# Kernel tuning notes

Measured on AMD Instinct MI355X. Metric: run time of the kernel, lower is better.

Reference implementation:

```python
import jax, jax.numpy as jnp
import numpy as np

B, DM, DC, H = 16384, 1024, 8, 256  # batch, MRI feat dim, clinical feat dim, hidden_dim


def setup_inputs() -> dict:
    key = jax.random.key(0)
    ks = jax.random.split(key, 16)
    f = lambda k, s: jax.random.normal(k, s, dtype=jnp.float32)
    return {
        # encoder outputs (4 MRI modalities @1024-d, clinical @8-d)
        'feat_t1': f(ks[0], (B, DM)), 'feat_t1c': f(ks[1], (B, DM)),
        'feat_t2': f(ks[2], (B, DM)), 'feat_flair': f(ks[3], (B, DM)),
        'feat_cl': f(ks[4], (B, DC)),
        # per-modality projection Linears (MRI ones stacked: same math as 4 separate Linears)
        'Wp_mri': f(ks[5], (4, H, DM)) * 0.02, 'bp_mri': jnp.zeros((4, H), jnp.float32),
        'Wp_cl': f(ks[6], (H, DC)) * 0.02, 'bp_cl': jnp.zeros((H,), jnp.float32),
        # attention MLP: Linear(256,64) -> Tanh -> Linear(64,1)
        'Wa1': f(ks[7], (64, H)) * 0.02, 'ba1': jnp.zeros((64,), jnp.float32),
        'Wa2': f(ks[8], (1, 64)) * 0.02, 'ba2': jnp.zeros((1,), jnp.float32),
        # classifier: 256->128 LN ReLU -> 128->64 LN ReLU -> 64->1 (num_class-1)
        'Wc1': f(ks[9], (128, H)) * 0.02, 'bc1': jnp.zeros((128,), jnp.float32),
        'g1': jnp.ones((128,), jnp.float32), 'be1': jnp.zeros((128,), jnp.float32),
        'Wc2': f(ks[10], (64, 128)) * 0.02, 'bc2': jnp.zeros((64,), jnp.float32),
        'g2': jnp.ones((64,), jnp.float32), 'be2': jnp.zeros((64,), jnp.float32),
        'Wc3': f(ks[11], (1, 64)) * 0.02, 'bc3': jnp.zeros((1,), jnp.float32),
    }


def _ln(x, g, b, eps=1e-5):
    m = jnp.mean(x, axis=-1, keepdims=True)
    v = jnp.var(x, axis=-1, keepdims=True)
    return (x - m) * jax.lax.rsqrt(v + eps) * g + b


def reference(feat_t1, feat_t1c, feat_t2, feat_flair, feat_cl,
              Wp_mri, bp_mri, Wp_cl, bp_cl,
              Wa1, ba1, Wa2, ba2,
              Wc1, bc1, g1, be1, Wc2, bc2, g2, be2, Wc3, bc3):
    mri = jnp.stack([feat_t1, feat_t1c, feat_t2, feat_flair], axis=1)  # [B,4,DM]
    pm = jnp.einsum('bmd,mhd->bmh', mri, Wp_mri) + bp_mri              # [B,4,H] per-modality Linear
    pc = feat_cl @ Wp_cl.T + bp_cl                                     # [B,H]
    proj = jnp.concatenate([pm, pc[:, None, :]], axis=1)               # [B,5,H] == torch.stack(proj_feats, dim=1)
    scores = jnp.tanh(proj @ Wa1.T + ba1) @ Wa2.T + ba2                # [B,5,1]
    attn_weights = jax.nn.softmax(scores, axis=1)                      # softmax over modalities
    fused = jnp.sum(attn_weights * proj, axis=1)                       # [B,H]
    h = jax.nn.relu(_ln(fused @ Wc1.T + bc1, g1, be1))                 # dropout is identity in eval
    h = jax.nn.relu(_ln(h @ Wc2.T + bc2, g2, be2))
    out = h @ Wc3.T + bc3                                              # [B,1]
    return out, attn_weights
```

## Files before the change

### kernel.cpp

```cpp
#include <hip/hip_runtime.h>
#include <math.h>

typedef unsigned short u16;
typedef unsigned int   u32;
typedef __bf16 bf16x8 __attribute__((ext_vector_type(8)));
typedef float  f32x4  __attribute__((ext_vector_type(4)));
typedef u16    u16x8  __attribute__((ext_vector_type(8)));
typedef u16    u16x4  __attribute__((ext_vector_type(4)));

#define B_TOT 16384
#define DM_   1024
#define H_    256

#define WS_SCORES 41943040
#define WS_WP     42270720
#define WS_WA1    44367872
#define WS_WC1    44400640
#define WS_WC2    44466176

__device__ __forceinline__ u16 f2bf(float f){
  __bf16 h = (__bf16)f;
  return __builtin_bit_cast(u16, h);
}
__device__ __forceinline__ float bf2f(u16 h){
  return __builtin_bit_cast(float, ((u32)h) << 16);
}
__device__ __forceinline__ u16x4 cvt4(f32x4 a){
  u16x4 h;
  #pragma unroll
  for (int j = 0; j < 4; j++) h[j] = f2bf(a[j]);
  return h;
}
__device__ __forceinline__ f32x4 mfma16(bf16x8 a, bf16x8 b, f32x4 c){
  return __builtin_amdgcn_mfma_f32_16x16x32_bf16(a, b, c, 0, 0, 0);
}
__device__ __forceinline__ void glds16(const void* g, void* l){
  __builtin_amdgcn_global_load_lds(
      (const __attribute__((address_space(1))) void*)g,
      (__attribute__((address_space(3))) void*)l, 16, 0, 0);
}

__global__ void k0_convert(const float* __restrict__ s0, u16* __restrict__ d0, int n0,
                           const float* __restrict__ s1, u16* __restrict__ d1, int n1,
                           const float* __restrict__ s2, u16* __restrict__ d2, int n2,
                           const float* __restrict__ s3, u16* __restrict__ d3, int n3)
{
  int total4 = (n0 + n1 + n2 + n3) >> 2;
  for (int i = blockIdx.x * blockDim.x + threadIdx.x; i < total4; i += gridDim.x * blockDim.x){
    int e = i << 2;
    const float* s; u16* d; int off;
    if (e < n0)            { s = s0; d = d0; off = e; }
    else if (e < n0+n1)    { s = s1; d = d1; off = e - n0; }
    else if (e < n0+n1+n2) { s = s2; d = d2; off = e - n0 - n1; }
    else                   { s = s3; d = d3; off = e - n0 - n1 - n2; }
    f32x4 f = *(const f32x4*)(s + off);
    *(u16x4*)(d + off) = cvt4(f);
  }
}

__global__ __launch_bounds__(256) void k1b_clin(
    const float* __restrict__ fcl, const float* __restrict__ Wpcl, const float* __restrict__ bpcl,
    const u16* __restrict__ Wa1bf, const float* __restrict__ ba1,
    const float* __restrict__ Wa2, const float* __restrict__ ba2,
    u16* __restrict__ proj, float* __restrict__ scores)
{
  __shared__ u16 pcs[4][16*264];
  const int tid = threadIdx.x, lane = tid & 63, wv = tid >> 6;
  const int l15 = lane & 15, l4 = lane >> 4;
  const int rbase = blockIdx.x * 64 + wv * 16;

  f32x4 wA[4], wB[4];
  f32x4 bp = *(const f32x4*)(bpcl + lane * 4);
  #pragma unroll
  for (int c = 0; c < 4; c++){
    wA[c] = *(const f32x4*)(Wpcl + (lane*4 + c) * 8);
    wB[c] = *(const f32x4*)(Wpcl + (lane*4 + c) * 8 + 4);
  }
  #pragma unroll 4
  for (int r = 0; r < 16; r++){
    int row = rbase + r;
    f32x4 fA = *(const f32x4*)(fcl + (size_t)row * 8);
    f32x4 fB = *(const f32x4*)(fcl + (size_t)row * 8 + 4);
    u16x4 h;
    #pragma unroll
    for (int c = 0; c < 4; c++){
      float v = bp[c] + fA[0]*wA[c][0] + fA[1]*wA[c][1] + fA[2]*wA[c][2] + fA[3]*wA[c][3]
                      + fB[0]*wB[c][0] + fB[1]*wB[c][1] + fB[2]*wB[c][2] + fB[3]*wB[c][3];
      h[c] = f2bf(v);
    }
    *(u16x4*)(proj + (size_t)row * 1280 + 1024 + lane * 4) = h;
    *(u16x4*)(&pcs[wv][r * 264 + lane * 4]) = h;
  }
  f32x4 at[4];
  #pragma unroll
  for (int nf = 0; nf < 4; nf++) at[nf] = f32x4{0.f,0.f,0.f,0.f};
  #pragma unroll
  for (int kk = 0; kk < 8; kk++){
    bf16x8 a = *(const bf16x8*)((const char*)&pcs[wv][0] + l15*528 + kk*64 + l4*16);
    #pragma unroll
    for (int nf = 0; nf < 4; nf++){
      bf16x8 b = *(const bf16x8*)((const char*)Wa1bf + (nf*16 + l15)*512 + kk*64 + l4*16);
      at[nf] = mfma16(a, b, at[nf]);
    }
  }
  float po[4] = {0.f,0.f,0.f,0.f};
  #pragma unroll
  for (int nf = 0; nf < 4; nf++){
    int col = nf*16 + l15;
    float bb = ba1[col], w2 = Wa2[col];
    #pragma unroll
    for (int rg = 0; rg < 4; rg++) po[rg] += tanhf(at[nf][rg] + bb) * w2;
  }
  #pragma unroll
  for (int rg = 0; rg < 4; rg++){
    #pragma unroll
    for (int d = 1; d < 16; d <<= 1) po[rg] += __shfl_xor(po[rg], d);
  }
  if (l15 == 0){
    float b2 = ba2[0];
    #pragma unroll
    for (int rg = 0; rg < 4; rg++)
      scores[(size_t)(rbase + l4*4 + rg) * 5 + 4] = po[rg] + b2;
  }
}

__global__ __launch_bounds__(512, 6) void k1_proj(
    const float* __restrict__ ft1, const float* __restrict__ ft1c,
    const float* __restrict__ ft2, const float* __restrict__ ftfl,
    const u16* __restrict__ Wpbf, const float* __restrict__ bpm,
    const u16* __restrict__ Wa1bf, const float* __restrict__ ba1,
    const float* __restrict__ Wa2, const float* __restrict__ ba2,
    u16* __restrict__ proj, float* __restrict__ scores)
{
  extern __shared__ char lds[];
  const int bid = blockIdx.x;
  const int mm = (bid & 7) >> 1;
  const int bx = ((bid >> 3) << 1) | (bid & 1);
  const int b0 = bx * 64;
  const int tid = threadIdx.x;
  const int lane = tid & 63;
  const int wv = tid >> 6;
  const int wm = wv >> 2, wn = wv & 3;
  const int l15 = lane & 15, l4 = lane >> 4;

  const float* Am = (mm == 0) ? ft1 : ((mm == 1) ? ft1c : ((mm == 2) ? ft2 : ftfl));
  const char*  Wm = (const char*)(Wpbf + (size_t)mm * (H_ * DM_));
  const char*  Ab8 = (const char*)Am;

  const int a_r = tid >> 3, a_c = tid & 7;
  const size_t a_src0 = (size_t)(b0 + a_r) * 4096 + (size_t)((a_c*16) ^ ((a_r & 7) << 4));
  const int a_dstw = (tid >> 6) * 1024;
  int w_pr[2], w_c[2]; size_t w_src0[2];
  #pragma unroll
  for (int i = 0; i < 2; i++){
    int q = i*512 + tid; w_pr[i] = q >> 3; w_c[i] = q & 7;
    int zp = (w_c[i]*16) ^ ((w_pr[i] & 7) << 4);
    int col = 2*w_pr[i] + (zp >> 6);
    w_src0[i] = (size_t)col * 2048 + (size_t)(zp & 63);
  }

  f32x4 acc[2][4];
  #pragma unroll
  for (int i = 0; i < 2; i++)
    #pragma unroll
    for (int j = 0; j < 4; j++) acc[i][j] = f32x4{0.f,0.f,0.f,0.f};

  int a_off[2], w_off[4];
  #pragma unroll
  for (int mf = 0; mf < 2; mf++){
    int r = wm*32 + mf*16 + l15;
    a_off[mf] = r*128 + ((l4*32) ^ ((r & 7) << 4));
  }
  int a_off2[2];
  #pragma unroll
  for (int mf = 0; mf < 2; mf++){
    int r = wm*32 + mf*16 + l15;
    a_off2[mf] = r*128 + (((l4*32) + 16) ^ ((r & 7) << 4));
  }
  #pragma unroll
  for (int nf = 0; nf < 4; nf++){
    int col = wn*64 + nf*16 + l15;
    int p = col >> 1, qq = col & 1;
    w_off[nf] = p*128 + (((qq*64) + l4*16) ^ ((p & 7) << 4));
  }

  glds16(Ab8 + a_src0, lds + a_dstw);
  #pragma unroll
  for (int i = 0; i < 2; i++)
    glds16(Wm + w_src0[i], lds + 16384 + i*8192 + a_dstw);
  __syncthreads();

  for (int kt = 0; kt < 32; ++kt){
    const int cur = kt & 1;
    if (kt < 31){
      const int nb = cur ^ 1;
      glds16(Ab8 + a_src0 + (size_t)(kt+1)*128, lds + nb*8192 + a_dstw);
      #pragma unroll
      for (int i = 0; i < 2; i++)
        glds16(Wm + w_src0[i] + (size_t)(kt+1)*64, lds + 16384 + nb*16384 + i*8192 + a_dstw);
    }
    const char* Abuf = lds + cur*8192;
    const char* Wbuf = lds + 16384 + cur*16384;
    bf16x8 af[2];
    #pragma unroll
    for (int mf = 0; mf < 2; mf++){
      f32x4 a0 = *(const f32x4*)(Abuf + a_off[mf]);
      f32x4 a1 = *(const f32x4*)(Abuf + a_off2[mf]);
      bf16x8 h;
      #pragma unroll
      for (int j = 0; j < 4; j++){ h[j] = (__bf16)a0[j]; h[4+j] = (__bf16)a1[j]; }
      af[mf] = h;
    }
    #pragma unroll
    for (int nf = 0; nf < 4; nf++){
      bf16x8 wfr = *(const bf16x8*)(Wbuf + w_off[nf]);
      #pragma unroll
      for (int mf = 0; mf < 2; mf++)
        acc[mf][nf] = mfma16(af[mf], wfr, acc[mf][nf]);
    }
    __syncthreads();
  }

  {
    float bias[4];
    #pragma unroll
    for (int nf = 0; nf < 4; nf++) bias[nf] = bpm[mm*256 + wn*64 + nf*16 + l15];
    #pragma unroll
    for (int mf = 0; mf < 2; mf++){
      #pragma unroll
      for (int nf = 0; nf < 4; nf++){
        int cc = wn*64 + nf*16 + l15;
        #pragma unroll
        for (int rg = 0; rg < 4; rg++){
          int r = wm*32 + mf*16 + l4*4 + rg;
          *(u16*)(lds + r*512 + ((cc*2) ^ ((r & 7) << 4))) = f2bf(acc[mf][nf][rg] + bias[nf]);
        }
      }
    }
  }
  __syncthreads();

  #pragma unroll
  for (int i = 0; i < 4; i++){
    int q = i*512 + tid;
    int r = q >> 5, c = q & 31;
    u16x8 v = *(const u16x8*)(lds + r*512 + ((c*16) ^ ((r & 7) << 4)));
    *(u16x8*)((char*)proj + (size_t)(b0 + r) * 2560 + mm*512 + c*16) = v;
  }
  if (wv < 4){
    f32x4 a2[4];
    #pragma unroll
    for (int nf = 0; nf < 4; nf++) a2[nf] = f32x4{0.f,0.f,0.f,0.f};
    #pragma unroll
    for (int kk = 0; kk < 8; kk++){
      int kb = kk*64 + l4*16;
      int r = wv*16 + l15;
      bf16x8 afr = *(const bf16x8*)(lds + r*512 + (kb ^ ((r & 7) << 4)));
      #pragma unroll
      for (int nf = 0; nf < 4; nf++){
        int n = nf*16 + l15;
        bf16x8 bfr = *(const bf16x8*)((const char*)Wa1bf + n*512 + kb);
        a2[nf] = mfma16(afr, bfr, a2[nf]);
      }
    }
    float p0 = 0.f, p1 = 0.f, p2 = 0.f, p3 = 0.f;
    #pragma unroll
    for (int nf = 0; nf < 4; nf++){
      int n = nf*16 + l15;
      float w2 = Wa2[n], bn = ba1[n];
      p0 += tanhf(a2[nf][0] + bn) * w2;
      p1 += tanhf(a2[nf][1] + bn) * w2;
      p2 += tanhf(a2[nf][2] + bn) * w2;
      p3 += tanhf(a2[nf][3] + bn) * w2;
    }
    #pragma unroll
    for (int d = 1; d < 16; d <<= 1){
      p0 += __shfl_xor(p0, d); p1 += __shfl_xor(p1, d);
      p2 += __shfl_xor(p2, d); p3 += __shfl_xor(p3, d);
    }
    if (l15 == 0){
      float bav = ba2[0];
      int rb = wv*16 + l4*4;
      scores[(size_t)(b0 + rb + 0)*5 + mm] = p0 + bav;
      scores[(size_t)(b0 + rb + 1)*5 + mm] = p1 + bav;
      scores[(size_t)(b0 + rb + 2)*5 + mm] = p2 + bav;
      scores[(size_t)(b0 + rb + 3)*5 + mm] = p3 + bav;
    }
  }
}

__global__ __launch_bounds__(256) void k2_cls(
    const u16* __restrict__ proj, const float* __restrict__ scores,
    const u16* __restrict__ Wc1bf, const u16* __restrict__ Wc2bf,
    const float* __restrict__ bc1, const float* __restrict__ g1, const float* __restrict__ be1,
    const float* __restrict__ bc2, const float* __restrict__ g2, const float* __restrict__ be2,
    const float* __restrict__ Wc3, const float* __restrict__ bc3,
    float* __restrict__ outp)
{
  __shared__ u16 h1s[4][16*136];
  const int tid = threadIdx.x, lane = tid & 63, wv = tid >> 6;
  const int l15 = lane & 15, l4 = lane >> 4;
  const int b0 = blockIdx.x * 64;
  const int rowA = b0 + wv*16 + l15;

  const float* sc = scores + (size_t)rowA * 5;
  float s0 = sc[0], s1 = sc[1], s2 = sc[2], s3 = sc[3], s4 = sc[4];
  float mx = fmaxf(fmaxf(fmaxf(s0, s1), fmaxf(s2, s3)), s4);
  float e0 = expf(s0-mx), e1 = expf(s1-mx), e2 = expf(s2-mx), e3 = expf(s3-mx), e4 = expf(s4-mx);
  float inv = 1.0f / (e0 + e1 + e2 + e3 + e4);
  float w0 = e0*inv, w1 = e1*inv, w2 = e2*inv, w3 = e3*inv, w4 = e4*inv;
  if (l4 == 0){
    float* ap = outp + B_TOT + (size_t)rowA * 5;
    ap[0] = w0; ap[1] = w1; ap[2] = w2; ap[3] = w3; ap[4] = w4;
  }

  bf16x8 af[8];
  const u16* pr = proj + (size_t)rowA * 1280 + l4*8;
  #pragma unroll
  for (int kk = 0; kk < 8; kk++){
    u16x8 p0v = *(const u16x8*)(pr + kk*32);
    u16x8 p1v = *(const u16x8*)(pr + 256  + kk*32);
    u16x8 p2v = *(const u16x8*)(pr + 512  + kk*32);
    u16x8 p3v = *(const u16x8*)(pr + 768  + kk*32);
    u16x8 p4v = *(const u16x8*)(pr + 1024 + kk*32);
    bf16x8 a;
    #pragma unroll
    for (int j = 0; j < 8; j++)
      a[j] = (__bf16)(w0*bf2f(p0v[j]) + w1*bf2f(p1v[j]) + w2*bf2f(p2v[j])
                    + w3*bf2f(p3v[j]) + w4*bf2f(p4v[j]));
    af[kk] = a;
  }

  f32x4 acc1[8];
  #pragma unroll
  for (int of = 0; of < 8; of++) acc1[of] = f32x4{0.f,0.f,0.f,0.f};
  #pragma unroll
  for (int kk = 0; kk < 8; kk++){
    #pragma unroll
    for (int of = 0; of < 8; of++){
      bf16x8 b = *(const bf16x8*)((const char*)Wc1bf + (of*16 + l15)*512 + kk*64 + l4*16);
      acc1[of] = mfma16(af[kk], b, acc1[of]);
    }
  }
  float sum1[4] = {0.f,0.f,0.f,0.f};
  #pragma unroll
  for (int of = 0; of < 8; of++){
    float bb = bc1[of*16 + l15];
    #pragma unroll
    for (int rg = 0; rg < 4; rg++){ acc1[of][rg] += bb; sum1[rg] += acc1[of][rg]; }
  }
  #pragma unroll
  for (int rg = 0; rg < 4; rg++){
    #pragma unroll
    for (int d = 1; d < 16; d <<= 1) sum1[rg] += __shfl_xor(sum1[rg], d);
  }
  float vs1[4] = {0.f,0.f,0.f,0.f};
  float mean1[4];
  #pragma unroll
  for (int rg = 0; rg < 4; rg++) mean1[rg] = sum1[rg] * 0.0078125f;
  #pragma unroll
  for (int of = 0; of < 8; of++)
    #pragma unroll
    for (int rg = 0; rg < 4; rg++){ float dd = acc1[of][rg] - mean1[rg]; vs1[rg] += dd*dd; }
  #pragma unroll
  for (int rg = 0; rg < 4; rg++){
    #pragma unroll
    for (int d = 1; d < 16; d <<= 1) vs1[rg] += __shfl_xor(vs1[rg], d);
  }
  float is1[4];
  #pragma unroll
  for (int rg = 0; rg < 4; rg++) is1[rg] = rsqrtf(vs1[rg] * 0.0078125f + 1e-5f);
  #pragma unroll
  for (int of = 0; of < 8; of++){
    int col = of*16 + l15;
    float gg = g1[col], bb = be1[col];
    #pragma unroll
    for (int rg = 0; rg < 4; rg++){
      float h = fmaxf((acc1[of][rg] - mean1[rg]) * is1[rg] * gg + bb, 0.f);
      h1s[wv][(l4*4 + rg)*136 + col] = f2bf(h);
    }
  }

  f32x4 acc2[4];
  #pragma unroll
  for (int of = 0; of < 4; of++) acc2[of] = f32x4{0.f,0.f,0.f,0.f};
  #pragma unroll
  for (int kk = 0; kk < 4; kk++){
    bf16x8 a2 = *(const bf16x8*)((const char*)&h1s[wv][0] + l15*272 + kk*64 + l4*16);
    #pragma unroll
    for (int of = 0; of < 4; of++){
      bf16x8 b = *(const bf16x8*)((const char*)Wc2bf + (of*16 + l15)*256 + kk*64 + l4*16);
      acc2[of] = mfma16(a2, b, acc2[of]);
    }
  }
  float sum2[4] = {0.f,0.f,0.f,0.f};
  #pragma unroll
  for (int of = 0; of < 4; of++){
    float bb = bc2[of*16 + l15];
    #pragma unroll
    for (int rg = 0; rg < 4; rg++){ acc2[of][rg] += bb; sum2[rg] += acc2[of][rg]; }
  }
  #pragma unroll
  for (int rg = 0; rg < 4; rg++){
    #pragma unroll
    for (int d = 1; d < 16; d <<= 1) sum2[rg] += __shfl_xor(sum2[rg], d);
  }
  float mean2[4], vs2[4] = {0.f,0.f,0.f,0.f};
  #pragma unroll
  for (int rg = 0; rg < 4; rg++) mean2[rg] = sum2[rg] * 0.015625f;
  #pragma unroll
  for (int of = 0; of < 4; of++)
    #pragma unroll
    for (int rg = 0; rg < 4; rg++){ float dd = acc2[of][rg] - mean2[rg]; vs2[rg] += dd*dd; }
  #pragma unroll
  for (int rg = 0; rg < 4; rg++){
    #pragma unroll
    for (int d = 1; d < 16; d <<= 1) vs2[rg] += __shfl_xor(vs2[rg], d);
  }
  float po[4] = {0.f,0.f,0.f,0.f};
  #pragma unroll
  for (int of = 0; of < 4; of++){
    int col = of*16 + l15;
    float gg = g2[col], bb = be2[col], w3c = Wc3[col];
    #pragma unroll
    for (int rg = 0; rg < 4; rg++){
      float is2 = rsqrtf(vs2[rg] * 0.015625f + 1e-5f);
      float h = fmaxf((acc2[of][rg] - mean2[rg]) * is2 * gg + bb, 0.f);
      po[rg] += h * w3c;
    }
  }
  #pragma unroll
  for (int rg = 0; rg < 4; rg++){
    #pragma unroll
    for (int d = 1; d < 16; d <<= 1) po[rg] += __shfl_xor(po[rg], d);
  }
  if (l15 == 0){
    float b3 = bc3[0];
    #pragma unroll
    for (int rg = 0; rg < 4; rg++)
      outp[b0 + wv*16 + l4*4 + rg] = po[rg] + b3;
  }
}

extern "C" void kernel_launch(void* const* d_in, const int* in_sizes, int n_in,
                              void* d_out, int out_size, void* d_ws, size_t ws_size,
                              hipStream_t stream)
{
  (void)in_sizes; (void)n_in; (void)out_size; (void)ws_size;
  const float* ft1  = (const float*)d_in[0];
  const float* ft1c = (const float*)d_in[1];
  const float* ft2  = (const float*)d_in[2];
  const float* ftfl = (const float*)d_in[3];
  const float* fcl  = (const float*)d_in[4];
  const float* Wpmri= (const float*)d_in[5];
  const float* bpm  = (const float*)d_in[6];
  const float* Wpcl = (const float*)d_in[7];
  const float* bpcl = (const float*)d_in[8];
  const float* Wa1  = (const float*)d_in[9];
  const float* ba1  = (const float*)d_in[10];
  const float* Wa2  = (const float*)d_in[11];
  const float* ba2  = (const float*)d_in[12];
  const float* Wc1  = (const float*)d_in[13];
  const float* bc1  = (const float*)d_in[14];
  const float* g1   = (const float*)d_in[15];
  const float* be1  = (const float*)d_in[16];
  const float* Wc2  = (const float*)d_in[17];
  const float* bc2  = (const float*)d_in[18];
  const float* g2   = (const float*)d_in[19];
  const float* be2  = (const float*)d_in[20];
  const float* Wc3  = (const float*)d_in[21];
  const float* bc3  = (const float*)d_in[22];
  float* outp = (float*)d_out;
  char* ws = (char*)d_ws;

  u16*   proj   = (u16*)(ws);
  float* scores = (float*)(ws + WS_SCORES);
  u16*   Wpbf   = (u16*)(ws + WS_WP);
  u16*   Wa1bf  = (u16*)(ws + WS_WA1);
  u16*   Wc1bf  = (u16*)(ws + WS_WC1);
  u16*   Wc2bf  = (u16*)(ws + WS_WC2);

  k0_convert<<<dim3(512), dim3(256), 0, stream>>>(
      Wpmri, Wpbf, 4 * H_ * DM_,
      Wa1,  Wa1bf, 64 * H_,
      Wc1,  Wc1bf, 128 * H_,
      Wc2,  Wc2bf, 64 * 128);

  k1b_clin<<<dim3(256), dim3(256), 0, stream>>>(
      fcl, Wpcl, bpcl, Wa1bf, ba1, Wa2, ba2, proj, scores);

  k1_proj<<<dim3(1024), dim3(512), 49152, stream>>>(
      ft1, ft1c, ft2, ftfl, Wpbf, bpm, Wa1bf, ba1, Wa2, ba2, proj, scores);

  k2_cls<<<dim3(256), dim3(256), 0, stream>>>(
      proj, scores, Wc1bf, Wc2bf, bc1, g1, be1, bc2, g2, be2, Wc3, bc3, outp);
}
```

Baseline: 149.3 us.

## Triple-buffer k1_proj global-to-LDS loads with one barrier per k-step

Converts the projection GEMM's double-buffered LDS pipeline into a three-stage ring. Each k-step waits with a partial vmcnt and issues a single barrier, replacing the trailing __syncthreads per iteration. It also batches the W fragment reads before the MFMAs and raises wave priority around them. The LDS footprint grows from 48KB to 72KB per block and launch bounds drop to 4 blocks, trading occupancy for deeper prefetch.

```diff
diff --git a/kernel.cpp b/kernel.cpp
--- a/kernel.cpp
+++ b/kernel.cpp
@@ -124,7 +124,7 @@
   }
 }
 
-__global__ __launch_bounds__(512, 6) void k1_proj(
+__global__ __launch_bounds__(512, 4) void k1_proj(
     const float* __restrict__ ft1, const float* __restrict__ ft1c,
     const float* __restrict__ ft2, const float* __restrict__ ftfl,
     const u16* __restrict__ Wpbf, const float* __restrict__ bpm,
@@ -150,12 +150,12 @@
   const int a_r = tid >> 3, a_c = tid & 7;
   const size_t a_src0 = (size_t)(b0 + a_r) * 4096 + (size_t)((a_c*16) ^ ((a_r & 7) << 4));
   const int a_dstw = (tid >> 6) * 1024;
-  int w_pr[2], w_c[2]; size_t w_src0[2];
+  size_t w_src0[2];
   #pragma unroll
   for (int i = 0; i < 2; i++){
-    int q = i*512 + tid; w_pr[i] = q >> 3; w_c[i] = q & 7;
-    int zp = (w_c[i]*16) ^ ((w_pr[i] & 7) << 4);
-    int col = 2*w_pr[i] + (zp >> 6);
+    int q = i*512 + tid; int pr = q >> 3, c = q & 7;
+    int zp = (c*16) ^ ((pr & 7) << 4);
+    int col = 2*pr + (zp >> 6);
     w_src0[i] = (size_t)col * 2048 + (size_t)(zp & 63);
   }
 
@@ -165,16 +165,11 @@
     #pragma unroll
     for (int j = 0; j < 4; j++) acc[i][j] = f32x4{0.f,0.f,0.f,0.f};
 
-  int a_off[2], w_off[4];
+  int a_off[2], a_off2[2], w_off[4];
   #pragma unroll
   for (int mf = 0; mf < 2; mf++){
     int r = wm*32 + mf*16 + l15;
-    a_off[mf] = r*128 + ((l4*32) ^ ((r & 7) << 4));
-  }
-  int a_off2[2];
-  #pragma unroll
-  for (int mf = 0; mf < 2; mf++){
-    int r = wm*32 + mf*16 + l15;
+    a_off[mf]  = r*128 + ((l4*32) ^ ((r & 7) << 4));
     a_off2[mf] = r*128 + (((l4*32) + 16) ^ ((r & 7) << 4));
   }
   #pragma unroll
@@ -184,23 +179,17 @@
     w_off[nf] = p*128 + (((qq*64) + l4*16) ^ ((p & 7) << 4));
   }
 
-  glds16(Ab8 + a_src0, lds + a_dstw);
-  #pragma unroll
-  for (int i = 0; i < 2; i++)
-    glds16(Wm + w_src0[i], lds + 16384 + i*8192 + a_dstw);
-  __syncthreads();
-
-  for (int kt = 0; kt < 32; ++kt){
-    const int cur = kt & 1;
-    if (kt < 31){
-      const int nb = cur ^ 1;
-      glds16(Ab8 + a_src0 + (size_t)(kt+1)*128, lds + nb*8192 + a_dstw);
-      #pragma unroll
-      for (int i = 0; i < 2; i++)
-        glds16(Wm + w_src0[i] + (size_t)(kt+1)*64, lds + 16384 + nb*16384 + i*8192 + a_dstw);
-    }
-    const char* Abuf = lds + cur*8192;
-    const char* Wbuf = lds + 16384 + cur*16384;
+  auto stage = [&](int t){
+    int bc = t % 3;
+    glds16(Ab8 + a_src0 + (size_t)t * 128, lds + bc*8192 + a_dstw);
+    #pragma unroll
+    for (int i = 0; i < 2; i++)
+      glds16(Wm + w_src0[i] + (size_t)t * 64, lds + 24576 + bc*16384 + i*8192 + a_dstw);
+  };
+  auto compute = [&](int t){
+    int bc = t % 3;
+    const char* Abuf = lds + bc*8192;
+    const char* Wbuf = lds + 24576 + bc*16384;
     bf16x8 af[2];
     #pragma unroll
     for (int mf = 0; mf < 2; mf++){
@@ -211,15 +200,35 @@
       for (int j = 0; j < 4; j++){ h[j] = (__bf16)a0[j]; h[4+j] = (__bf16)a1[j]; }
       af[mf] = h;
     }
+    bf16x8 wfr[4];
+    #pragma unroll
+    for (int nf = 0; nf < 4; nf++) wfr[nf] = *(const bf16x8*)(Wbuf + w_off[nf]);
+    __builtin_amdgcn_s_setprio(1);
     #pragma unroll
     for (int nf = 0; nf < 4; nf++){
-      bf16x8 wfr = *(const bf16x8*)(Wbuf + w_off[nf]);
       #pragma unroll
       for (int mf = 0; mf < 2; mf++)
-        acc[mf][nf] = mfma16(af[mf], wfr, acc[mf][nf]);
-    }
-    __syncthreads();
-  }
+        acc[mf][nf] = mfma16(af[mf], wfr[nf], acc[mf][nf]);
+    }
+    __builtin_amdgcn_s_setprio(0);
+  };
+
+  stage(0);
+  stage(1);
+
+  for (int kt = 0; kt < 31; ++kt){
+    asm volatile("s_waitcnt vmcnt(3)" ::: "memory");
+    __builtin_amdgcn_s_barrier();
+    __builtin_amdgcn_sched_barrier(0);
+    if (kt + 2 < 32) stage(kt + 2);
+    compute(kt);
+  }
+  asm volatile("s_waitcnt vmcnt(0)" ::: "memory");
+  __builtin_amdgcn_s_barrier();
+  __builtin_amdgcn_sched_barrier(0);
+  compute(31);
+
+  __syncthreads();
 
   {
     float bias[4];
@@ -480,6 +489,8 @@
   u16*   Wc1bf  = (u16*)(ws + WS_WC1);
   u16*   Wc2bf  = (u16*)(ws + WS_WC2);
 
+  (void)hipFuncSetAttribute((const void*)k1_proj, hipFuncAttributeMaxDynamicSharedMemorySize, 73728);
+
   k0_convert<<<dim3(512), dim3(256), 0, stream>>>(
       Wpmri, Wpbf, 4 * H_ * DM_,
       Wa1,  Wa1bf, 64 * H_,
@@ -489,7 +500,7 @@
   k1b_clin<<<dim3(256), dim3(256), 0, stream>>>(
       fcl, Wpcl, bpcl, Wa1bf, ba1, Wa2, ba2, proj, scores);
 
-  k1_proj<<<dim3(1024), dim3(512), 49152, stream>>>(
+  k1_proj<<<dim3(1024), dim3(512), 73728, stream>>>(
       ft1, ft1c, ft2, ftfl, Wpbf, bpm, Wa1bf, ba1, Wa2, ba2, proj, scores);
 
   k2_cls<<<dim3(256), dim3(256), 0, stream>>>(
```

Result: faster. 141.6 us (-5.2%).

## Load GEMM operands directly into registers instead of staging through LDS

Applied to the files above, without the earlier changes.

The projection GEMM mainloop stops staging A and W tiles through double-buffered LDS with global_load_lds and per-iteration barriers. Each wave now loads its own MFMA fragments straight from global memory into a two-deep register prefetch pipeline, and the K loop is fully unrolled. LDS shrinks to a static 32KB used only for the epilogue, and launch bounds drop to 4 waves per SIMD to make room for the extra registers. The trade-off is that operands shared across waves are no longer reused through LDS: each wave issues its own global loads, and the row-strided accesses coalesce less well, which raises traffic to L2 and global memory.

```diff
diff --git a/kernel.cpp b/kernel.cpp
--- a/kernel.cpp
+++ b/kernel.cpp
@@ -33,11 +33,6 @@
 }
 __device__ __forceinline__ f32x4 mfma16(bf16x8 a, bf16x8 b, f32x4 c){
   return __builtin_amdgcn_mfma_f32_16x16x32_bf16(a, b, c, 0, 0, 0);
-}
-__device__ __forceinline__ void glds16(const void* g, void* l){
-  __builtin_amdgcn_global_load_lds(
-      (const __attribute__((address_space(1))) void*)g,
-      (__attribute__((address_space(3))) void*)l, 16, 0, 0);
 }
 
 __global__ void k0_convert(const float* __restrict__ s0, u16* __restrict__ d0, int n0,
@@ -124,7 +119,7 @@
   }
 }
 
-__global__ __launch_bounds__(512, 6) void k1_proj(
+__global__ __launch_bounds__(512, 4) void k1_proj(
     const float* __restrict__ ft1, const float* __restrict__ ft1c,
     const float* __restrict__ ft2, const float* __restrict__ ftfl,
     const u16* __restrict__ Wpbf, const float* __restrict__ bpm,
@@ -132,7 +127,7 @@
     const float* __restrict__ Wa2, const float* __restrict__ ba2,
     u16* __restrict__ proj, float* __restrict__ scores)
 {
-  extern __shared__ char lds[];
+  __shared__ char lds[32768];
   const int bid = blockIdx.x;
   const int mm = (bid & 7) >> 1;
   const int bx = ((bid >> 3) << 1) | (bid & 1);
@@ -144,82 +139,62 @@
   const int l15 = lane & 15, l4 = lane >> 4;
 
   const float* Am = (mm == 0) ? ft1 : ((mm == 1) ? ft1c : ((mm == 2) ? ft2 : ftfl));
-  const char*  Wm = (const char*)(Wpbf + (size_t)mm * (H_ * DM_));
-  const char*  Ab8 = (const char*)Am;
-
-  const int a_r = tid >> 3, a_c = tid & 7;
-  const size_t a_src0 = (size_t)(b0 + a_r) * 4096 + (size_t)((a_c*16) ^ ((a_r & 7) << 4));
-  const int a_dstw = (tid >> 6) * 1024;
-  int w_pr[2], w_c[2]; size_t w_src0[2];
-  #pragma unroll
-  for (int i = 0; i < 2; i++){
-    int q = i*512 + tid; w_pr[i] = q >> 3; w_c[i] = q & 7;
-    int zp = (w_c[i]*16) ^ ((w_pr[i] & 7) << 4);
-    int col = 2*w_pr[i] + (zp >> 6);
-    w_src0[i] = (size_t)col * 2048 + (size_t)(zp & 63);
-  }
-
+  const u16*   Wm = Wpbf + (size_t)mm * (H_ * DM_);
+
+  const float* pA0 = Am + (size_t)(b0 + wm*32 + l15) * DM_ + l4*8;
+  const float* pA1 = pA0 + 16 * DM_;
+  const u16*   pW  = Wm + (size_t)(wn*64 + l15) * DM_ + l4*8;
+
+  f32x4 rA[2][4];
+  u16x8 rW[2][4];
   f32x4 acc[2][4];
   #pragma unroll
   for (int i = 0; i < 2; i++)
     #pragma unroll
     for (int j = 0; j < 4; j++) acc[i][j] = f32x4{0.f,0.f,0.f,0.f};
 
-  int a_off[2], w_off[4];
-  #pragma unroll
-  for (int mf = 0; mf < 2; mf++){
-    int r = wm*32 + mf*16 + l15;
-    a_off[mf] = r*128 + ((l4*32) ^ ((r & 7) << 4));
-  }
-  int a_off2[2];
-  #pragma unroll
-  for (int mf = 0; mf < 2; mf++){
-    int r = wm*32 + mf*16 + l15;
-    a_off2[mf] = r*128 + (((l4*32) + 16) ^ ((r & 7) << 4));
-  }
-  #pragma unroll
-  for (int nf = 0; nf < 4; nf++){
-    int col = wn*64 + nf*16 + l15;
-    int p = col >> 1, qq = col & 1;
-    w_off[nf] = p*128 + (((qq*64) + l4*16) ^ ((p & 7) << 4));
-  }
-
-  glds16(Ab8 + a_src0, lds + a_dstw);
-  #pragma unroll
-  for (int i = 0; i < 2; i++)
-    glds16(Wm + w_src0[i], lds + 16384 + i*8192 + a_dstw);
-  __syncthreads();
-
-  for (int kt = 0; kt < 32; ++kt){
-    const int cur = kt & 1;
-    if (kt < 31){
-      const int nb = cur ^ 1;
-      glds16(Ab8 + a_src0 + (size_t)(kt+1)*128, lds + nb*8192 + a_dstw);
-      #pragma unroll
-      for (int i = 0; i < 2; i++)
-        glds16(Wm + w_src0[i] + (size_t)(kt+1)*64, lds + 16384 + nb*16384 + i*8192 + a_dstw);
-    }
-    const char* Abuf = lds + cur*8192;
-    const char* Wbuf = lds + 16384 + cur*16384;
+  #define K1_ISSUE(c) do{                                     \
+    const int p_ = (c) & 1;                                   \
+    const float* a0_ = pA0 + (c)*32;                          \
+    const float* a1_ = pA1 + (c)*32;                          \
+    rA[p_][0] = *(const f32x4*)(a0_);                         \
+    rA[p_][1] = *(const f32x4*)(a0_ + 4);                     \
+    rA[p_][2] = *(const f32x4*)(a1_);                         \
+    rA[p_][3] = *(const f32x4*)(a1_ + 4);                     \
+    const u16* w_ = pW + (c)*32;                              \
+    rW[p_][0] = *(const u16x8*)(w_);                          \
+    rW[p_][1] = *(const u16x8*)(w_ + 16*DM_);                 \
+    rW[p_][2] = *(const u16x8*)(w_ + 32*DM_);                 \
+    rW[p_][3] = *(const u16x8*)(w_ + 48*DM_);                 \
+  } while(0)
+
+  K1_ISSUE(0);
+  K1_ISSUE(1);
+
+  #pragma unroll
+  for (int c = 0; c < 32; ++c){
+    const int p = c & 1;
     bf16x8 af[2];
     #pragma unroll
     for (int mf = 0; mf < 2; mf++){
-      f32x4 a0 = *(const f32x4*)(Abuf + a_off[mf]);
-      f32x4 a1 = *(const f32x4*)(Abuf + a_off2[mf]);
+      f32x4 a0 = rA[p][mf*2], a1 = rA[p][mf*2 + 1];
       bf16x8 h;
       #pragma unroll
       for (int j = 0; j < 4; j++){ h[j] = (__bf16)a0[j]; h[4+j] = (__bf16)a1[j]; }
       af[mf] = h;
     }
+    bf16x8 wf[4];
+    #pragma unroll
+    for (int nf = 0; nf < 4; nf++) wf[nf] = __builtin_bit_cast(bf16x8, rW[p][nf]);
+    if (c + 2 < 32) K1_ISSUE(c + 2);
     #pragma unroll
     for (int nf = 0; nf < 4; nf++){
-      bf16x8 wfr = *(const bf16x8*)(Wbuf + w_off[nf]);
       #pragma unroll
       for (int mf = 0; mf < 2; mf++)
-        acc[mf][nf] = mfma16(af[mf], wfr, acc[mf][nf]);
-    }
-    __syncthreads();
-  }
+        acc[mf][nf] = mfma16(af[mf], wf[nf], acc[mf][nf]);
+    }
+  }
+  #undef K1_ISSUE
 
   {
     float bias[4];
@@ -243,9 +218,9 @@
   #pragma unroll
   for (int i = 0; i < 4; i++){
     int q = i*512 + tid;
-    int r = q >> 5, c = q & 31;
-    u16x8 v = *(const u16x8*)(lds + r*512 + ((c*16) ^ ((r & 7) << 4)));
-    *(u16x8*)((char*)proj + (size_t)(b0 + r) * 2560 + mm*512 + c*16) = v;
+    int r = q >> 5, cc = q & 31;
+    u16x8 v = *(const u16x8*)(lds + r*512 + ((cc*16) ^ ((r & 7) << 4)));
+    *(u16x8*)((char*)proj + (size_t)(b0 + r) * 2560 + mm*512 + cc*16) = v;
   }
   if (wv < 4){
     f32x4 a2[4];
@@ -489,7 +464,7 @@
   k1b_clin<<<dim3(256), dim3(256), 0, stream>>>(
       fcl, Wpcl, bpcl, Wa1bf, ba1, Wa2, ba2, proj, scores);
 
-  k1_proj<<<dim3(1024), dim3(512), 49152, stream>>>(
+  k1_proj<<<dim3(1024), dim3(512), 0, stream>>>(
       ft1, ft1c, ft2, ftfl, Wpbf, bpm, Wa1bf, ba1, Wa2, ba2, proj, scores);
 
   k2_cls<<<dim3(256), dim3(256), 0, stream>>>(
```

After: 288.0 us. 92.9% more time.
